# Optimization experiments

Measured on AMD Instinct MI355X. Metric: run time of the kernel, lower is better.

The kernel has to match this reference:

```python
import jax, jax.numpy as jnp
import numpy as np
import math

N_HEAD = 32
HEAD_DIM = 64
ROTARY_DIM = 32
ROTARY_BASE = 10000.0
NEG_INF = -10000.0


def _rope_cos_sin(seqlen):
    # RotaryEmbedding._update_cos_sin_cache: inv_freq over even indices of rotary_dim
    inv_freq = 1.0 / (ROTARY_BASE ** (jnp.arange(0, ROTARY_DIM, 2, dtype=jnp.float32) / ROTARY_DIM))
    t = jnp.arange(seqlen, dtype=jnp.float32)
    freqs = jnp.outer(t, inv_freq)  # [s, rd/2]
    return jnp.cos(freqs), jnp.sin(freqs)


def _apply_rotary(t, cos, sin):
    # t: [b, s, h, d]; GPT-NeoX half-rotation on first ROTARY_DIM dims, pass-through rest
    half = ROTARY_DIM // 2
    x1 = t[..., :half]
    x2 = t[..., half:ROTARY_DIM]
    x_pass = t[..., ROTARY_DIM:]
    c = cos[:, None, :]  # [s, 1, rd/2] -> broadcasts over (b, s, h, rd/2)
    s_ = sin[:, None, :]
    return jnp.concatenate([x1 * c - x2 * s_, x1 * s_ + x2 * c, x_pass], axis=-1)


def setup_inputs() -> dict:
    key = jax.random.key(0)
    k1, k2, k3, k4, k5 = jax.random.split(key, 5)
    b, s, e = 2, 2048, 2048
    return {
        "x": jax.random.normal(k1, (b, s, e), dtype=jnp.float32),
        "Wqkv": jax.random.normal(k2, (e, 3 * e), dtype=jnp.float32) * 0.02,
        "bqkv": jax.random.normal(k3, (3 * e,), dtype=jnp.float32) * 0.02,
        "Wout": jax.random.normal(k4, (e, e), dtype=jnp.float32) * 0.02,
        "bout": jax.random.normal(k5, (e,), dtype=jnp.float32) * 0.02,
    }


def reference(x, Wqkv, bqkv, Wout, bout):
    b, s, e = x.shape
    # QKV projection -> [b, s, 3, h, d]
    qkv = (x @ Wqkv + bqkv).reshape(b, s, 3, N_HEAD, HEAD_DIM)
    cos, sin = _rope_cos_sin(s)
    q = _apply_rotary(qkv[:, :, 0], cos, sin)
    k = _apply_rotary(qkv[:, :, 1], cos, sin)
    v = qkv[:, :, 2]
    # Attention (SelfAttention/CrossAttention math, fp32, materialized scores)
    scale = 1.0 / math.sqrt(HEAD_DIM)
    scores = jnp.einsum('bthd,bshd->bhts', q, k * scale)  # [b, h, s, s]
    rows = jnp.arange(s)[:, None]
    cols = jnp.arange(s)[None, :]
    causal_mask = cols > rows  # seqlen_q == seqlen_k
    scores = jnp.where(causal_mask, NEG_INF, scores)
    attn = jax.nn.softmax(scores, axis=-1)
    out = jnp.einsum('bhts,bshd->bthd', attn, v).reshape(b, s, e)
    return out @ Wout + bout
```

## Files before the change

kernel.cpp:

```cpp
#include <hip/hip_runtime.h>


typedef _Float16 half8 __attribute__((ext_vector_type(8)));
typedef _Float16 half4 __attribute__((ext_vector_type(4)));
typedef float floatx4 __attribute__((ext_vector_type(4)));

#define GLD_LDS16(gp, sp)                                        \
  __builtin_amdgcn_global_load_lds(                              \
      (__attribute__((address_space(1))) void*)(gp),             \
      (__attribute__((address_space(3))) void*)(sp), 16, 0, 0)

__device__ __forceinline__ floatx4 mfma16(half8 a, half8 b, floatx4 c) {
  return __builtin_amdgcn_mfma_f32_16x16x32_f16(a, b, c, 0, 0, 0);
}
__device__ __forceinline__ floatx4 mfma16k16(half4 a, half4 b, floatx4 c) {
  return __builtin_amdgcn_mfma_f32_16x16x16f16(a, b, c, 0, 0, 0);
}

__global__ __launch_bounds__(256) void cvt_x_kernel(const float* __restrict__ x,
                                                    _Float16* __restrict__ xh) {
  int idx = blockIdx.x * 256 + threadIdx.x;
  const floatx4* p = (const floatx4*)x + (size_t)idx * 2;
  floatx4 a = p[0], b = p[1];
  half8 o;
#pragma unroll
  for (int j = 0; j < 4; ++j) { o[j] = (_Float16)a[j]; o[4 + j] = (_Float16)b[j]; }
  *((half8*)xh + idx) = o;
}

__global__ __launch_bounds__(256) void cvt_wt_kernel(const float* __restrict__ W,
                                                     _Float16* __restrict__ Wt,
                                                     int Kd, int Nd) {
  __shared__ float tile[64][65];
  int n0 = blockIdx.x * 64, k0 = blockIdx.y * 64;
  int tid = threadIdx.x;
#pragma unroll
  for (int it = 0; it < 4; ++it) {
    int r = (tid >> 4) + it * 16;
    int c = (tid & 15) * 4;
    floatx4 v = *(const floatx4*)(W + (size_t)(k0 + r) * Nd + n0 + c);
    tile[r][c + 0] = v[0]; tile[r][c + 1] = v[1];
    tile[r][c + 2] = v[2]; tile[r][c + 3] = v[3];
  }
  __syncthreads();
#pragma unroll
  for (int it = 0; it < 2; ++it) {
    int r = (tid >> 3) + it * 32;
    int c = (tid & 7) * 8;
    half8 o;
#pragma unroll
    for (int j = 0; j < 8; ++j) o[j] = (_Float16)tile[c + j][r];
    *(half8*)(Wt + (size_t)(n0 + r) * Kd + k0 + c) = o;
  }
}

__global__ __launch_bounds__(512, 2) void gemm_qkv_kernel(
    const _Float16* __restrict__ A, const _Float16* __restrict__ Bt,
    const float* __restrict__ bias,
    _Float16* __restrict__ Qd, _Float16* __restrict__ Kkd,
    _Float16* __restrict__ Vd) {
  __shared__ __align__(16) _Float16 sA[2][16384];
  __shared__ __align__(16) _Float16 sB[2][12288];
  constexpr int KD = 2048;
  constexpr int NT = KD / 64;

  int tid = threadIdx.x, w = tid >> 6, l = tid & 63;
  int lr = l & 15, quad = l >> 4;
  int wr = w >> 1, wc = w & 1;
  int m0 = blockIdx.y * 256, n0 = blockIdx.x * 192;

  int csw0 = ((quad) ^ (lr & 7)) * 8;
  int csw1 = ((quad + 4) ^ (lr & 7)) * 8;

  const _Float16* pA[4];
  const _Float16* pB[3];
  {
    int rl = l >> 3;
    int cs = ((l & 7) ^ rl) * 8;
#pragma unroll
    for (int jj = 0; jj < 4; ++jj)
      pA[jj] = A + (size_t)(m0 + w * 32 + jj * 8 + rl) * KD + cs;
#pragma unroll
    for (int jj = 0; jj < 3; ++jj)
      pB[jj] = Bt + (size_t)(n0 + w * 24 + jj * 8 + rl) * KD + cs;
  }

#define STAGE_ALL(BUF, KT)                                                   \
  _Pragma("unroll") for (int jj = 0; jj < 4; ++jj)                           \
    GLD_LDS16(pA[jj] + (KT), &sA[BUF][(w * 32 + jj * 8) * 64]);              \
  _Pragma("unroll") for (int jj = 0; jj < 3; ++jj)                           \
    GLD_LDS16(pB[jj] + (KT), &sB[BUF][(w * 24 + jj * 8) * 64]);

  floatx4 z4 = {0.f, 0.f, 0.f, 0.f};
  floatx4 acc[4][6];
#pragma unroll
  for (int i = 0; i < 4; ++i)
#pragma unroll
    for (int j = 0; j < 6; ++j) acc[i][j] = z4;

  STAGE_ALL(0, 0);
  asm volatile("s_waitcnt vmcnt(0)" ::: "memory");
  __builtin_amdgcn_s_barrier();

  half8 af[4][2], bf[6][2];
#pragma unroll 2
  for (int t = 0; t < NT; ++t) {
    int buf = t & 1, nbuf = buf ^ 1;
    if (t + 1 < NT) { STAGE_ALL(nbuf, (t + 1) * 64); }
#pragma unroll
    for (int j = 0; j < 6; ++j) {
      int row_ = wc * 96 + j * 16 + lr;
      bf[j][0] = *(const half8*)&sB[buf][row_ * 64 + csw0];
      bf[j][1] = *(const half8*)&sB[buf][row_ * 64 + csw1];
    }
#pragma unroll
    for (int i = 0; i < 4; ++i) {
      int row_ = wr * 64 + i * 16 + lr;
      af[i][0] = *(const half8*)&sA[buf][row_ * 64 + csw0];
      af[i][1] = *(const half8*)&sA[buf][row_ * 64 + csw1];
    }
    __builtin_amdgcn_s_setprio(1);
#pragma unroll
    for (int j = 0; j < 6; ++j)
#pragma unroll
      for (int ks = 0; ks < 2; ++ks)
#pragma unroll
        for (int i = 0; i < 4; ++i)
          acc[i][j] = mfma16(af[i][ks], bf[j][ks], acc[i][j]);
    __builtin_amdgcn_s_setprio(0);
    asm volatile("s_waitcnt vmcnt(0)" ::: "memory");
    __builtin_amdgcn_s_barrier();
  }

  float bj[6];
#pragma unroll
  for (int j = 0; j < 6; ++j) bj[j] = bias[n0 + wc * 96 + j * 16 + lr];
  float freq = __expf(-(float)lr * 0.57564627324851148f);
#pragma unroll
  for (int j = 0; j < 6; ++j) {
    int cb = wc * 96 + j * 16;
    int cg = n0 + cb;
    int which = cg >> 11;
    int d0 = cb & 63;
    int hh = (cg & 2047) >> 6;
    if (which == 2) {
      int dd = d0 + lr;
#pragma unroll
      for (int i = 0; i < 4; ++i) {
        int m = m0 + wr * 64 + i * 16 + quad * 4;
        int bb = m >> 11, tt = m & 2047;
        half4 h;
#pragma unroll
        for (int r = 0; r < 4; ++r) h[r] = (_Float16)(acc[i][j][r] + bj[j]);
        *(half4*)&Vd[(((size_t)(bb * 32 + hh)) * 64 + dd) * 2048 + tt] = h;
      }
    } else if (d0 == 0) {
      _Float16* dst = which ? Kkd : Qd;
#pragma unroll
      for (int i = 0; i < 4; ++i)
#pragma unroll
        for (int r = 0; r < 4; ++r) {
          int m = m0 + wr * 64 + i * 16 + quad * 4 + r;
          int bb = m >> 11, tt = m & 2047;
          float sn, cs2;
          __sincosf((float)tt * freq, &sn, &cs2);
          float x1 = acc[i][j][r] + bj[j];
          float x2 = acc[i][j + 1][r] + bj[j + 1];
          _Float16* row = dst + ((size_t)(bb * 32 + hh) * 2048 + (size_t)tt) * 64;
          row[lr] = (_Float16)(x1 * cs2 - x2 * sn);
          row[lr + 16] = (_Float16)(x1 * sn + x2 * cs2);
        }
    } else if (d0 >= 32) {
      _Float16* dst = which ? Kkd : Qd;
#pragma unroll
      for (int i = 0; i < 4; ++i)
#pragma unroll
        for (int r = 0; r < 4; ++r) {
          int m = m0 + wr * 64 + i * 16 + quad * 4 + r;
          int bb = m >> 11, tt = m & 2047;
          _Float16* row = dst + ((size_t)(bb * 32 + hh) * 2048 + (size_t)tt) * 64;
          row[d0 + lr] = (_Float16)(acc[i][j][r] + bj[j]);
        }
    }
  }
#undef STAGE_ALL
}

template <int MODE>
__global__ __launch_bounds__(256) void gemm_f16_kernel(
    const _Float16* __restrict__ A, const _Float16* __restrict__ Bt,
    const float* __restrict__ bias, int Kd, int Nd,
    _Float16* __restrict__ Qd, _Float16* __restrict__ Kkd,
    _Float16* __restrict__ Vd, float* __restrict__ Co) {
  __shared__ __align__(16) _Float16 sA[128 * 64];
  __shared__ __align__(16) _Float16 sB[128 * 64];
  int tid = threadIdx.x, w = tid >> 6, l = tid & 63;
  int lr = l & 15, lq = l >> 4;
  int m0 = blockIdx.y * 128, n0 = blockIdx.x * 128;
  int wrow = (w >> 1) * 64, wcol = (w & 1) * 64;

  floatx4 z4 = {0.f, 0.f, 0.f, 0.f};
  floatx4 acc[4][4];
#pragma unroll
  for (int i = 0; i < 4; ++i)
#pragma unroll
    for (int j = 0; j < 4; ++j) acc[i][j] = z4;

  int srow = l >> 3;
  int slot = (l & 7) ^ srow;
  const _Float16* aG = A + (size_t)(m0 + w * 32 + srow) * Kd + slot * 8;
  const _Float16* bG = Bt + (size_t)(n0 + w * 32 + srow) * Kd + slot * 8;
  _Float16* sAw = &sA[w * 2048];
  _Float16* sBw = &sB[w * 2048];

  for (int kt = 0; kt < Kd; kt += 64) {
#pragma unroll
    for (int t = 0; t < 4; ++t) {
      GLD_LDS16(aG + (size_t)t * 8 * Kd + kt, sAw + t * 512);
      GLD_LDS16(bG + (size_t)t * 8 * Kd + kt, sBw + t * 512);
    }
    __syncthreads();
#pragma unroll
    for (int ks = 0; ks < 2; ++ks) {
      half8 af[4], bf[4];
#pragma unroll
      for (int i = 0; i < 4; ++i) {
        int ar = wrow + i * 16 + lr;
        int br = wcol + i * 16 + lr;
        int sl = (((ks << 2) | lq) ^ (lr & 7)) * 8;
        af[i] = *(const half8*)&sA[ar * 64 + sl];
        bf[i] = *(const half8*)&sB[br * 64 + sl];
      }
#pragma unroll
      for (int i = 0; i < 4; ++i)
#pragma unroll
        for (int j = 0; j < 4; ++j) acc[i][j] = mfma16(af[i], bf[j], acc[i][j]);
    }
    __syncthreads();
  }

  if (MODE == 0) {
    int which = n0 >> 11;
    float bj[4];
#pragma unroll
    for (int j = 0; j < 4; ++j) bj[j] = bias[n0 + wcol + j * 16 + lr];
    int hh = ((n0 & 2047) + wcol) >> 6;
    if (which == 2) {
#pragma unroll
      for (int j = 0; j < 4; ++j) {
        int dd = j * 16 + lr;
#pragma unroll
        for (int i = 0; i < 4; ++i) {
          int m = m0 + wrow + i * 16 + lq * 4;
          int bb = m >> 11, t = m & 2047;
          half4 h;
#pragma unroll
          for (int r = 0; r < 4; ++r) h[r] = (_Float16)(acc[i][j][r] + bj[j]);
          *(half4*)&Vd[(((size_t)(bb * 32 + hh)) * 64 + dd) * 2048 + t] = h;
        }
      }
    } else {
      _Float16* dst = which ? Kkd : Qd;
      float freq = __expf(-(float)lr * 0.57564627324851148f);
#pragma unroll
      for (int i = 0; i < 4; ++i)
#pragma unroll
        for (int r = 0; r < 4; ++r) {
          int m = m0 + wrow + i * 16 + lq * 4 + r;
          int bb = m >> 11, t = m & 2047;
          float sn, cs;
          __sincosf((float)t * freq, &sn, &cs);
          float x1 = acc[i][0][r] + bj[0];
          float x2 = acc[i][1][r] + bj[1];
          _Float16* row = dst + ((size_t)(bb * 32 + hh) * 2048 + (size_t)t) * 64;
          row[lr]      = (_Float16)(x1 * cs - x2 * sn);
          row[lr + 16] = (_Float16)(x1 * sn + x2 * cs);
          row[lr + 32] = (_Float16)(acc[i][2][r] + bj[2]);
          row[lr + 48] = (_Float16)(acc[i][3][r] + bj[3]);
        }
    }
  } else {
#pragma unroll
    for (int j = 0; j < 4; ++j) {
      int n = n0 + wcol + j * 16 + lr;
      float bj = bias[n];
#pragma unroll
      for (int i = 0; i < 4; ++i)
#pragma unroll
        for (int r = 0; r < 4; ++r) {
          int m = m0 + wrow + i * 16 + lq * 4 + r;
          Co[(size_t)m * Nd + n] = acc[i][j][r] + bj;
        }
    }
  }
}

__global__ __launch_bounds__(256) void attn_kernel(
    const _Float16* __restrict__ Q, const _Float16* __restrict__ Kk,
    const _Float16* __restrict__ Vt, _Float16* __restrict__ O) {
  constexpr int S = 2048;
  int bh = blockIdx.x;
  int qt = 15 - blockIdx.y;
  int bb = bh >> 5, hh = bh & 31;
  const _Float16* Qb = Q + (size_t)bh * S * 64;
  const _Float16* Kb = Kk + (size_t)bh * S * 64;
  const _Float16* Vb = Vt + (size_t)bh * 64 * S;

  __shared__ __align__(16) _Float16 sK[128 * 72];
  __shared__ __align__(16) _Float16 sVt[64 * 136];

  int tid = threadIdx.x, w = tid >> 6, l = tid & 63;
  int lr = l & 15, quad = l >> 4;

  int rk = tid >> 3, ck = (tid & 7) * 8;
  int rv = tid >> 4, cv = (tid & 15) * 8;
  const _Float16* Kst = Kb + (size_t)rk * 64 + ck;
  const _Float16* Vst = Vb + (size_t)rv * S + cv;

  floatx4 z4 = {0.f, 0.f, 0.f, 0.f};
  int q0 = qt * 128;

  half8 qf[2][2];
#pragma unroll
  for (int qtl = 0; qtl < 2; ++qtl)
#pragma unroll
    for (int ks = 0; ks < 2; ++ks) {
      half8 v = *(const half8*)(Qb + (size_t)(q0 + w * 32 + qtl * 16 + lr) * 64 +
                                ks * 32 + quad * 8);
      qf[qtl][ks] = v * (_Float16)0.18033688f;
    }

  floatx4 Oa[4][2];
  float m_i[2] = {-1e30f, -1e30f}, l_i[2] = {0.f, 0.f};
#pragma unroll
  for (int dt = 0; dt < 4; ++dt)
#pragma unroll
    for (int qtl = 0; qtl < 2; ++qtl) Oa[dt][qtl] = z4;

  half8 kpre[4], vpre[4];
#pragma unroll
  for (int it = 0; it < 4; ++it) {
    kpre[it] = *(const half8*)(Kst + (size_t)it * 32 * 64);
    vpre[it] = *(const half8*)(Vst + (size_t)it * 16 * S);
  }

  for (int jt = 0; jt <= qt; ++jt) {
#pragma unroll
    for (int it = 0; it < 4; ++it) {
      *(half8*)&sK[(rk + it * 32) * 72 + ck] = kpre[it];
      *(half8*)&sVt[(rv + it * 16) * 136 + cv] = vpre[it];
    }
    if (jt < qt) {
      int kv1 = (jt + 1) * 128;
#pragma unroll
      for (int it = 0; it < 4; ++it) {
        kpre[it] = *(const half8*)(Kst + (size_t)(kv1 + it * 32) * 64);
        vpre[it] = *(const half8*)(Vst + kv1 + (size_t)it * 16 * S);
      }
    }
    __syncthreads();

    floatx4 Sa[2][8];
#pragma unroll
    for (int qtl = 0; qtl < 2; ++qtl)
#pragma unroll
      for (int kvt = 0; kvt < 8; ++kvt) Sa[qtl][kvt] = z4;
    __builtin_amdgcn_s_setprio(1);
#pragma unroll
    for (int ks = 0; ks < 2; ++ks) {
#pragma unroll
      for (int kvt = 0; kvt < 8; ++kvt) {
        half8 kf = *(const half8*)&sK[(kvt * 16 + lr) * 72 + ks * 32 + quad * 8];
        Sa[0][kvt] = mfma16(kf, qf[0][ks], Sa[0][kvt]);
        Sa[1][kvt] = mfma16(kf, qf[1][ks], Sa[1][kvt]);
      }
    }
    __builtin_amdgcn_s_setprio(0);

    if (jt == qt) {
#pragma unroll
      for (int qtl = 0; qtl < 2; ++qtl) {
        int q_loc = w * 32 + qtl * 16 + lr;
#pragma unroll
        for (int kvt = 0; kvt < 8; ++kvt) {
          int kv_base = kvt * 16 + quad * 4;
#pragma unroll
          for (int r = 0; r < 4; ++r)
            if (kv_base + r > q_loc) Sa[qtl][kvt][r] = -1e30f;
        }
      }
    }

#pragma unroll
    for (int qtl = 0; qtl < 2; ++qtl) {
      float mx = Sa[qtl][0][0];
#pragma unroll
      for (int kvt = 0; kvt < 8; ++kvt)
#pragma unroll
        for (int r = 0; r < 4; ++r) mx = fmaxf(mx, Sa[qtl][kvt][r]);
      mx = fmaxf(mx, __shfl_xor(mx, 16));
      mx = fmaxf(mx, __shfl_xor(mx, 32));
      float mnew = fmaxf(m_i[qtl], mx);
      float alpha = __builtin_amdgcn_exp2f(m_i[qtl] - mnew);
      m_i[qtl] = mnew;
      float rs = 0.f;
#pragma unroll
      for (int kvt = 0; kvt < 8; ++kvt)
#pragma unroll
        for (int r = 0; r < 4; ++r) {
          float p = __builtin_amdgcn_exp2f(Sa[qtl][kvt][r] - mnew);
          Sa[qtl][kvt][r] = p;
          rs += p;
        }
      rs += __shfl_xor(rs, 16);
      rs += __shfl_xor(rs, 32);
      l_i[qtl] = l_i[qtl] * alpha + rs;
#pragma unroll
      for (int dt = 0; dt < 4; ++dt) Oa[dt][qtl] *= alpha;
    }

    __builtin_amdgcn_s_setprio(1);
#pragma unroll
    for (int kvt = 0; kvt < 8; ++kvt) {
      half4 vf[4];
#pragma unroll
      for (int dt = 0; dt < 4; ++dt)
        vf[dt] = *(const half4*)&sVt[(dt * 16 + lr) * 136 + kvt * 16 + quad * 4];
      half4 pf[2];
#pragma unroll
      for (int qtl = 0; qtl < 2; ++qtl) {
        pf[qtl][0] = (_Float16)Sa[qtl][kvt][0];
        pf[qtl][1] = (_Float16)Sa[qtl][kvt][1];
        pf[qtl][2] = (_Float16)Sa[qtl][kvt][2];
        pf[qtl][3] = (_Float16)Sa[qtl][kvt][3];
      }
#pragma unroll
      for (int dt = 0; dt < 4; ++dt)
#pragma unroll
        for (int qtl = 0; qtl < 2; ++qtl)
          Oa[dt][qtl] = mfma16k16(vf[dt], pf[qtl], Oa[dt][qtl]);
    }
    __builtin_amdgcn_s_setprio(0);
    __syncthreads();
  }

  float inv0 = 1.0f / l_i[0], inv1 = 1.0f / l_i[1];
#pragma unroll
  for (int dt = 0; dt < 4; ++dt)
#pragma unroll
    for (int qtl = 0; qtl < 2; ++qtl) {
      float inv = qtl ? inv1 : inv0;
      floatx4 o = Oa[dt][qtl];
      half4 hv;
      hv[0] = (_Float16)(o[0] * inv); hv[1] = (_Float16)(o[1] * inv);
      hv[2] = (_Float16)(o[2] * inv); hv[3] = (_Float16)(o[3] * inv);
      *(half4*)&sK[(w * 32 + qtl * 16 + lr) * 72 + dt * 16 + quad * 4] = hv;
    }
  __syncthreads();
#pragma unroll
  for (int it = 0; it < 2; ++it) {
    int row = (tid >> 2) + it * 64;
    int t = q0 + row;
    _Float16* orow = O + ((size_t)(bb * 2048 + t)) * 2048 + hh * 64;
#pragma unroll
    for (int cc = 0; cc < 2; ++cc) {
      int col = (tid & 3) * 16 + cc * 8;
      *(half8*)(orow + col) = *(const half8*)&sK[row * 72 + col];
    }
  }
}

extern "C" void kernel_launch(void* const* d_in, const int* in_sizes, int n_in,
                              void* d_out, int out_size, void* d_ws, size_t ws_size,
                              hipStream_t stream) {
  (void)in_sizes; (void)n_in; (void)out_size; (void)ws_size;
  const float* x = (const float*)d_in[0];
  const float* Wqkv = (const float*)d_in[1];
  const float* bqkv = (const float*)d_in[2];
  const float* Wout = (const float*)d_in[3];
  const float* bout = (const float*)d_in[4];
  float* out = (float*)d_out;
  char* ws = (char*)d_ws;

  _Float16* xh    = (_Float16*)(ws + 0);
  _Float16* wqkvt = (_Float16*)(ws + 16777216);
  _Float16* Oh    = (_Float16*)(ws + 16777216);
  _Float16* Qh    = (_Float16*)(ws + 41943040);
  _Float16* Kh    = (_Float16*)(ws + 58720256);
  _Float16* Vth   = (_Float16*)(ws + 75497472);
  _Float16* woutt = (_Float16*)(ws + 92274688);

  cvt_x_kernel<<<4096, 256, 0, stream>>>(x, xh);
  cvt_wt_kernel<<<dim3(96, 32), 256, 0, stream>>>(Wqkv, wqkvt, 2048, 6144);
  cvt_wt_kernel<<<dim3(32, 32), 256, 0, stream>>>(Wout, woutt, 2048, 2048);
  gemm_qkv_kernel<<<dim3(32, 16), 512, 0, stream>>>(xh, wqkvt, bqkv, Qh, Kh, Vth);
  attn_kernel<<<dim3(64, 16), 256, 0, stream>>>(Qh, Kh, Vth, Oh);
  gemm_f16_kernel<1><<<dim3(16, 32), 256, 0, stream>>>(
      Oh, woutt, bout, 2048, 2048, nullptr, nullptr, nullptr, out);
}
```

Measured before the change: 386.3 us.

## Double-buffer output GEMM with 256x128 tiles and restructure attention softmax loop

```diff
diff --git a/kernel.cpp b/kernel.cpp
--- a/kernel.cpp
+++ b/kernel.cpp
@@ -186,18 +186,40 @@
 #undef STAGE_ALL
 }
 
-template <int MODE>
-__global__ __launch_bounds__(256) void gemm_f16_kernel(
+__global__ __launch_bounds__(512, 2) void gemm_out_kernel(
     const _Float16* __restrict__ A, const _Float16* __restrict__ Bt,
-    const float* __restrict__ bias, int Kd, int Nd,
-    _Float16* __restrict__ Qd, _Float16* __restrict__ Kkd,
-    _Float16* __restrict__ Vd, float* __restrict__ Co) {
-  __shared__ __align__(16) _Float16 sA[128 * 64];
-  __shared__ __align__(16) _Float16 sB[128 * 64];
+    const float* __restrict__ bias, float* __restrict__ Co) {
+  __shared__ __align__(16) _Float16 sA[2][16384];
+  __shared__ __align__(16) _Float16 sB[2][8192];
+  constexpr int KD = 2048;
+  constexpr int NT = KD / 64;
+
   int tid = threadIdx.x, w = tid >> 6, l = tid & 63;
-  int lr = l & 15, lq = l >> 4;
-  int m0 = blockIdx.y * 128, n0 = blockIdx.x * 128;
-  int wrow = (w >> 1) * 64, wcol = (w & 1) * 64;
+  int lr = l & 15, quad = l >> 4;
+  int wr = w >> 1, wc = w & 1;
+  int m0 = blockIdx.y * 256, n0 = blockIdx.x * 128;
+
+  int csw0 = ((quad) ^ (lr & 7)) * 8;
+  int csw1 = ((quad + 4) ^ (lr & 7)) * 8;
+
+  const _Float16* pA[4];
+  const _Float16* pB[2];
+  {
+    int rl = l >> 3;
+    int cs = ((l & 7) ^ rl) * 8;
+#pragma unroll
+    for (int jj = 0; jj < 4; ++jj)
+      pA[jj] = A + (size_t)(m0 + w * 32 + jj * 8 + rl) * KD + cs;
+#pragma unroll
+    for (int jj = 0; jj < 2; ++jj)
+      pB[jj] = Bt + (size_t)(n0 + w * 16 + jj * 8 + rl) * KD + cs;
+  }
+
+#define STAGE_O(BUF, KT)                                                     \
+  _Pragma("unroll") for (int jj = 0; jj < 4; ++jj)                           \
+    GLD_LDS16(pA[jj] + (KT), &sA[BUF][(w * 32 + jj * 8) * 64]);              \
+  _Pragma("unroll") for (int jj = 0; jj < 2; ++jj)                           \
+    GLD_LDS16(pB[jj] + (KT), &sB[BUF][(w * 16 + jj * 8) * 64]);
 
   floatx4 z4 = {0.f, 0.f, 0.f, 0.f};
   floatx4 acc[4][4];
@@ -206,96 +228,56 @@
 #pragma unroll
     for (int j = 0; j < 4; ++j) acc[i][j] = z4;
 
-  int srow = l >> 3;
-  int slot = (l & 7) ^ srow;
-  const _Float16* aG = A + (size_t)(m0 + w * 32 + srow) * Kd + slot * 8;
-  const _Float16* bG = Bt + (size_t)(n0 + w * 32 + srow) * Kd + slot * 8;
-  _Float16* sAw = &sA[w * 2048];
-  _Float16* sBw = &sB[w * 2048];
-
-  for (int kt = 0; kt < Kd; kt += 64) {
-#pragma unroll
-    for (int t = 0; t < 4; ++t) {
-      GLD_LDS16(aG + (size_t)t * 8 * Kd + kt, sAw + t * 512);
-      GLD_LDS16(bG + (size_t)t * 8 * Kd + kt, sBw + t * 512);
-    }
-    __syncthreads();
-#pragma unroll
-    for (int ks = 0; ks < 2; ++ks) {
-      half8 af[4], bf[4];
-#pragma unroll
-      for (int i = 0; i < 4; ++i) {
-        int ar = wrow + i * 16 + lr;
-        int br = wcol + i * 16 + lr;
-        int sl = (((ks << 2) | lq) ^ (lr & 7)) * 8;
-        af[i] = *(const half8*)&sA[ar * 64 + sl];
-        bf[i] = *(const half8*)&sB[br * 64 + sl];
+  STAGE_O(0, 0);
+  asm volatile("s_waitcnt vmcnt(0)" ::: "memory");
+  __builtin_amdgcn_s_barrier();
+
+  half8 af[4][2], bf[4][2];
+#pragma unroll 2
+  for (int t = 0; t < NT; ++t) {
+    int buf = t & 1, nbuf = buf ^ 1;
+    if (t + 1 < NT) { STAGE_O(nbuf, (t + 1) * 64); }
+#pragma unroll
+    for (int j = 0; j < 4; ++j) {
+      int row_ = wc * 64 + j * 16 + lr;
+      bf[j][0] = *(const half8*)&sB[buf][row_ * 64 + csw0];
+      bf[j][1] = *(const half8*)&sB[buf][row_ * 64 + csw1];
+    }
+#pragma unroll
+    for (int i = 0; i < 4; ++i) {
+      int row_ = wr * 64 + i * 16 + lr;
+      af[i][0] = *(const half8*)&sA[buf][row_ * 64 + csw0];
+      af[i][1] = *(const half8*)&sA[buf][row_ * 64 + csw1];
+    }
+    __builtin_amdgcn_s_setprio(1);
+#pragma unroll
+    for (int j = 0; j < 4; ++j)
+#pragma unroll
+      for (int ks = 0; ks < 2; ++ks)
+#pragma unroll
+        for (int i = 0; i < 4; ++i)
+          acc[i][j] = mfma16(af[i][ks], bf[j][ks], acc[i][j]);
+    __builtin_amdgcn_s_setprio(0);
+    asm volatile("s_waitcnt vmcnt(0)" ::: "memory");
+    __builtin_amdgcn_s_barrier();
+  }
+
+#pragma unroll
+  for (int j = 0; j < 4; ++j) {
+    int n = n0 + wc * 64 + j * 16 + lr;
+    float bj = bias[n];
+#pragma unroll
+    for (int i = 0; i < 4; ++i)
+#pragma unroll
+      for (int r = 0; r < 4; ++r) {
+        int m = m0 + wr * 64 + i * 16 + quad * 4 + r;
+        Co[(size_t)m * 2048 + n] = acc[i][j][r] + bj;
       }
-#pragma unroll
-      for (int i = 0; i < 4; ++i)
-#pragma unroll
-        for (int j = 0; j < 4; ++j) acc[i][j] = mfma16(af[i], bf[j], acc[i][j]);
-    }
-    __syncthreads();
-  }
-
-  if (MODE == 0) {
-    int which = n0 >> 11;
-    float bj[4];
-#pragma unroll
-    for (int j = 0; j < 4; ++j) bj[j] = bias[n0 + wcol + j * 16 + lr];
-    int hh = ((n0 & 2047) + wcol) >> 6;
-    if (which == 2) {
-#pragma unroll
-      for (int j = 0; j < 4; ++j) {
-        int dd = j * 16 + lr;
-#pragma unroll
-        for (int i = 0; i < 4; ++i) {
-          int m = m0 + wrow + i * 16 + lq * 4;
-          int bb = m >> 11, t = m & 2047;
-          half4 h;
-#pragma unroll
-          for (int r = 0; r < 4; ++r) h[r] = (_Float16)(acc[i][j][r] + bj[j]);
-          *(half4*)&Vd[(((size_t)(bb * 32 + hh)) * 64 + dd) * 2048 + t] = h;
-        }
-      }
-    } else {
-      _Float16* dst = which ? Kkd : Qd;
-      float freq = __expf(-(float)lr * 0.57564627324851148f);
-#pragma unroll
-      for (int i = 0; i < 4; ++i)
-#pragma unroll
-        for (int r = 0; r < 4; ++r) {
-          int m = m0 + wrow + i * 16 + lq * 4 + r;
-          int bb = m >> 11, t = m & 2047;
-          float sn, cs;
-          __sincosf((float)t * freq, &sn, &cs);
-          float x1 = acc[i][0][r] + bj[0];
-          float x2 = acc[i][1][r] + bj[1];
-          _Float16* row = dst + ((size_t)(bb * 32 + hh) * 2048 + (size_t)t) * 64;
-          row[lr]      = (_Float16)(x1 * cs - x2 * sn);
-          row[lr + 16] = (_Float16)(x1 * sn + x2 * cs);
-          row[lr + 32] = (_Float16)(acc[i][2][r] + bj[2]);
-          row[lr + 48] = (_Float16)(acc[i][3][r] + bj[3]);
-        }
-    }
-  } else {
-#pragma unroll
-    for (int j = 0; j < 4; ++j) {
-      int n = n0 + wcol + j * 16 + lr;
-      float bj = bias[n];
-#pragma unroll
-      for (int i = 0; i < 4; ++i)
-#pragma unroll
-        for (int r = 0; r < 4; ++r) {
-          int m = m0 + wrow + i * 16 + lq * 4 + r;
-          Co[(size_t)m * Nd + n] = acc[i][j][r] + bj;
-        }
-    }
-  }
-}
-
-__global__ __launch_bounds__(256) void attn_kernel(
+  }
+#undef STAGE_O
+}
+
+__global__ __launch_bounds__(256, 4) void attn_kernel(
     const _Float16* __restrict__ Q, const _Float16* __restrict__ Kk,
     const _Float16* __restrict__ Vt, _Float16* __restrict__ O) {
   constexpr int S = 2048;
@@ -337,110 +319,102 @@
 #pragma unroll
     for (int qtl = 0; qtl < 2; ++qtl) Oa[dt][qtl] = z4;
 
-  half8 kpre[4], vpre[4];
-#pragma unroll
-  for (int it = 0; it < 4; ++it) {
+  half8 kpre[4];
+#pragma unroll
+  for (int it = 0; it < 4; ++it)
     kpre[it] = *(const half8*)(Kst + (size_t)it * 32 * 64);
-    vpre[it] = *(const half8*)(Vst + (size_t)it * 16 * S);
-  }
 
   for (int jt = 0; jt <= qt; ++jt) {
-#pragma unroll
-    for (int it = 0; it < 4; ++it) {
+    half8 vcur[4];
+#pragma unroll
+    for (int it = 0; it < 4; ++it)
+      vcur[it] = *(const half8*)(Vst + (size_t)jt * 128 + (size_t)it * 16 * S);
+#pragma unroll
+    for (int it = 0; it < 4; ++it)
       *(half8*)&sK[(rk + it * 32) * 72 + ck] = kpre[it];
-      *(half8*)&sVt[(rv + it * 16) * 136 + cv] = vpre[it];
-    }
     if (jt < qt) {
       int kv1 = (jt + 1) * 128;
 #pragma unroll
-      for (int it = 0; it < 4; ++it) {
+      for (int it = 0; it < 4; ++it)
         kpre[it] = *(const half8*)(Kst + (size_t)(kv1 + it * 32) * 64);
-        vpre[it] = *(const half8*)(Vst + kv1 + (size_t)it * 16 * S);
-      }
-    }
+    }
+#pragma unroll
+    for (int it = 0; it < 4; ++it)
+      *(half8*)&sVt[(rv + it * 16) * 136 + cv] = vcur[it];
     __syncthreads();
 
-    floatx4 Sa[2][8];
-#pragma unroll
-    for (int qtl = 0; qtl < 2; ++qtl)
-#pragma unroll
-      for (int kvt = 0; kvt < 8; ++kvt) Sa[qtl][kvt] = z4;
-    __builtin_amdgcn_s_setprio(1);
-#pragma unroll
-    for (int ks = 0; ks < 2; ++ks) {
-#pragma unroll
-      for (int kvt = 0; kvt < 8; ++kvt) {
-        half8 kf = *(const half8*)&sK[(kvt * 16 + lr) * 72 + ks * 32 + quad * 8];
-        Sa[0][kvt] = mfma16(kf, qf[0][ks], Sa[0][kvt]);
-        Sa[1][kvt] = mfma16(kf, qf[1][ks], Sa[1][kvt]);
-      }
-    }
-    __builtin_amdgcn_s_setprio(0);
-
-    if (jt == qt) {
-#pragma unroll
-      for (int qtl = 0; qtl < 2; ++qtl) {
+#pragma unroll
+    for (int qtl = 0; qtl < 2; ++qtl) {
+      floatx4 Sa[8];
+#pragma unroll
+      for (int kvt = 0; kvt < 8; ++kvt) Sa[kvt] = z4;
+      __builtin_amdgcn_s_setprio(1);
+#pragma unroll
+      for (int ks = 0; ks < 2; ++ks)
+#pragma unroll
+        for (int kvt = 0; kvt < 8; ++kvt) {
+          half8 kf = *(const half8*)&sK[(kvt * 16 + lr) * 72 + ks * 32 + quad * 8];
+          Sa[kvt] = mfma16(kf, qf[qtl][ks], Sa[kvt]);
+        }
+      __builtin_amdgcn_s_setprio(0);
+
+      if (jt == qt) {
         int q_loc = w * 32 + qtl * 16 + lr;
 #pragma unroll
         for (int kvt = 0; kvt < 8; ++kvt) {
           int kv_base = kvt * 16 + quad * 4;
 #pragma unroll
           for (int r = 0; r < 4; ++r)
-            if (kv_base + r > q_loc) Sa[qtl][kvt][r] = -1e30f;
+            if (kv_base + r > q_loc) Sa[kvt][r] = -1e30f;
         }
       }
-    }
-
-#pragma unroll
-    for (int qtl = 0; qtl < 2; ++qtl) {
-      float mx = Sa[qtl][0][0];
+
+      float mx = Sa[0][0];
 #pragma unroll
       for (int kvt = 0; kvt < 8; ++kvt)
 #pragma unroll
-        for (int r = 0; r < 4; ++r) mx = fmaxf(mx, Sa[qtl][kvt][r]);
+        for (int r = 0; r < 4; ++r) mx = fmaxf(mx, Sa[kvt][r]);
       mx = fmaxf(mx, __shfl_xor(mx, 16));
       mx = fmaxf(mx, __shfl_xor(mx, 32));
       float mnew = fmaxf(m_i[qtl], mx);
-      float alpha = __builtin_amdgcn_exp2f(m_i[qtl] - mnew);
+      if (!__all(mx <= m_i[qtl])) {
+        float alpha = __builtin_amdgcn_exp2f(m_i[qtl] - mnew);
+        l_i[qtl] *= alpha;
+#pragma unroll
+        for (int dt = 0; dt < 4; ++dt) Oa[dt][qtl] *= alpha;
+      }
       m_i[qtl] = mnew;
       float rs = 0.f;
 #pragma unroll
       for (int kvt = 0; kvt < 8; ++kvt)
 #pragma unroll
         for (int r = 0; r < 4; ++r) {
-          float p = __builtin_amdgcn_exp2f(Sa[qtl][kvt][r] - mnew);
-          Sa[qtl][kvt][r] = p;
+          float p = __builtin_amdgcn_exp2f(Sa[kvt][r] - mnew);
+          Sa[kvt][r] = p;
           rs += p;
         }
       rs += __shfl_xor(rs, 16);
       rs += __shfl_xor(rs, 32);
-      l_i[qtl] = l_i[qtl] * alpha + rs;
-#pragma unroll
-      for (int dt = 0; dt < 4; ++dt) Oa[dt][qtl] *= alpha;
-    }
-
-    __builtin_amdgcn_s_setprio(1);
-#pragma unroll
-    for (int kvt = 0; kvt < 8; ++kvt) {
-      half4 vf[4];
-#pragma unroll
-      for (int dt = 0; dt < 4; ++dt)
-        vf[dt] = *(const half4*)&sVt[(dt * 16 + lr) * 136 + kvt * 16 + quad * 4];
-      half4 pf[2];
-#pragma unroll
-      for (int qtl = 0; qtl < 2; ++qtl) {
-        pf[qtl][0] = (_Float16)Sa[qtl][kvt][0];
-        pf[qtl][1] = (_Float16)Sa[qtl][kvt][1];
-        pf[qtl][2] = (_Float16)Sa[qtl][kvt][2];
-        pf[qtl][3] = (_Float16)Sa[qtl][kvt][3];
+      l_i[qtl] += rs;
+
+      __builtin_amdgcn_s_setprio(1);
+#pragma unroll
+      for (int kvt = 0; kvt < 8; ++kvt) {
+        half4 vf[4];
+#pragma unroll
+        for (int dt = 0; dt < 4; ++dt)
+          vf[dt] = *(const half4*)&sVt[(dt * 16 + lr) * 136 + kvt * 16 + quad * 4];
+        half4 pf;
+        pf[0] = (_Float16)Sa[kvt][0];
+        pf[1] = (_Float16)Sa[kvt][1];
+        pf[2] = (_Float16)Sa[kvt][2];
+        pf[3] = (_Float16)Sa[kvt][3];
+#pragma unroll
+        for (int dt = 0; dt < 4; ++dt)
+          Oa[dt][qtl] = mfma16k16(vf[dt], pf, Oa[dt][qtl]);
       }
-#pragma unroll
-      for (int dt = 0; dt < 4; ++dt)
-#pragma unroll
-        for (int qtl = 0; qtl < 2; ++qtl)
-          Oa[dt][qtl] = mfma16k16(vf[dt], pf[qtl], Oa[dt][qtl]);
-    }
-    __builtin_amdgcn_s_setprio(0);
+      __builtin_amdgcn_s_setprio(0);
+    }
     __syncthreads();
   }
 
@@ -495,6 +469,5 @@
   cvt_wt_kernel<<<dim3(32, 32), 256, 0, stream>>>(Wout, woutt, 2048, 2048);
   gemm_qkv_kernel<<<dim3(32, 16), 512, 0, stream>>>(xh, wqkvt, bqkv, Qh, Kh, Vth);
   attn_kernel<<<dim3(64, 16), 256, 0, stream>>>(Qh, Kh, Vth, Oh);
-  gemm_f16_kernel<1><<<dim3(16, 32), 256, 0, stream>>>(
-      Oh, woutt, bout, 2048, 2048, nullptr, nullptr, nullptr, out);
-}
+  gemm_out_kernel<<<dim3(16, 16), 512, 0, stream>>>(Oh, woutt, bout, out);
+}
```

After: 389.8 us. About the same (+0.9%).
